# Optimization experiments

Hardware: AMD Instinct MI355X
Metric: run time of the kernel (lower is better)

The kernel has to match this reference:

```python
import jax, jax.numpy as jnp
import numpy as np

N, NUM_CLASSES, FEAT_DIM = 32768, 395, 512


def setup_inputs() -> dict:
    key = jax.random.key(0)
    k1, k2, k3, k4 = jax.random.split(key, 4)
    modal1_inputs = jax.random.normal(k1, (N, FEAT_DIM), dtype=jnp.float32)
    modal2_inputs = jax.random.normal(k2, (N, FEAT_DIM), dtype=jnp.float32)
    targets = jax.random.randint(k3, (N,), 0, NUM_CLASSES)
    # learned centers parameter: torch.rand -> uniform [0, 1)
    centers = jax.random.uniform(k4, (NUM_CLASSES, FEAT_DIM), dtype=jnp.float32)
    return {
        "modal1_inputs": modal1_inputs,
        "modal2_inputs": modal2_inputs,
        "centers": centers,
        "targets": targets,
    }


def _smooth_l1(a, b):
    # SmoothL1Loss with default beta=1.0, reduction='mean'
    d = jnp.abs(a - b)
    return jnp.mean(jnp.where(d < 1.0, 0.5 * d * d, d - 0.5))


def reference(modal1_inputs, modal2_inputs, centers, targets):
    num_classes = centers.shape[0]
    # Per-label mean (the original O(N^2) loop is exactly a segment mean
    # gathered back per sample).
    ones = jnp.ones((targets.shape[0],), dtype=modal1_inputs.dtype)
    counts = jax.ops.segment_sum(ones, targets, num_segments=num_classes)
    counts = jnp.maximum(counts, 1.0)  # empty classes never gathered
    sum1 = jax.ops.segment_sum(modal1_inputs, targets, num_segments=num_classes)
    sum2 = jax.ops.segment_sum(modal2_inputs, targets, num_segments=num_classes)
    centersR = (sum1 / counts[:, None])[targets]  # [N, D]
    centersT = (sum2 / counts[:, None])[targets]  # [N, D]
    gathered_centers = centers[targets]           # [N, D]
    loss = _smooth_l1(centersR, gathered_centers) + _smooth_l1(centersT, gathered_centers)
    return loss
```

## Files before the change

### kernel.cpp

```cpp
#include <hip/hip_runtime.h>

#define NS 32768
#define NC 395
#define FD 512
#define NEL (NC * FD)

#define RS 16
#define CT 16
#define COLS 32
#define ROWS_PB (NS / RS)
#define NW 8
#define LCAP 384

__device__ float g_part[2 * RS * NC * FD];
__device__ int   g_hist[RS * NC];

__global__ __launch_bounds__(512, 4)
void k_stream(const float* __restrict__ m1, const float* __restrict__ m2,
              const int* __restrict__ targets, float* __restrict__ out)
{
    const int bid = blockIdx.x;
    const int ct  = bid & (CT - 1);
    const int mod = (bid >> 4) & 1;
    const int rs  = bid >> 5;
    const int t   = threadIdx.x;
    const int w   = t >> 6;
    const int lane = t & 63;
    const int col  = lane & 31;
    const bool lo  = lane < 32;

    __shared__ float acc[NC * COLS];
    __shared__ int   lists[NW * LCAP];

    for (int i = t; i < NC * COLS; i += 512) acc[i] = 0.f;
    if (bid == 0 && t == 0) out[0] = 0.f;

    const int* tgt = targets + rs * ROWS_PB;
    int* mylist = &lists[w * LCAP];
    int cnt = 0;
    int nxt = tgt[lane];
    for (int it = 0; it < ROWS_PB / 64; ++it) {
        int c = nxt;
        if (it + 1 < ROWS_PB / 64) nxt = tgt[(it + 1) * 64 + lane];
        bool pred = ((c & 7) == w);
        unsigned long long mask = __ballot(pred);
        int pos = (int)__popcll(mask & ((1ull << lane) - 1ull));
        if (pred && cnt + pos < LCAP)
            mylist[cnt + pos] = (it * 64 + lane) | (c << 12);
        cnt += (int)__popcll(mask);
    }
    if (cnt > LCAP) cnt = LCAP;
    __syncthreads();

    const float* src = (mod ? m2 : m1) + (size_t)rs * ROWS_PB * FD + ct * COLS;
    const int npairs = (cnt + 1) >> 1;
    const int nbat   = (npairs + 3) >> 2;

    int ca0, cb0, ca1, cb1, ca2, cb2, ca3, cb3;
    int da0, db0, da1, db1, da2, db2, da3, db3;
    float v0, v1, v2, v3, u0, u1, u2, u3;

#define LOADP(CA, CB, V, P)                                              \
    {   int p_ = (P);                                                    \
        if (p_ < npairs) {                                               \
            int j0 = p_ << 1;                                            \
            int2 ee = *reinterpret_cast<const int2*>(&mylist[j0]);       \
            bool hb = (j0 + 1) < cnt;                                    \
            CA = ee.x >> 12;                                             \
            CB = hb ? (ee.y >> 12) : -1;                                 \
            int e = lo ? ee.x : (hb ? ee.y : ee.x);                      \
            V = src[(size_t)(e & 0xFFF) * FD + col];                     \
        } else { CA = -1; CB = -1; V = 0.f; }                            \
    }

#define RMWP(CA, CB, V)                                                  \
    if (CA >= 0) {                                                       \
        float v_ = V;                                                    \
        if (CA == CB) v_ += __shfl_xor(v_, 32, 64);                      \
        int cc = lo ? CA : CB;                                           \
        if (cc >= 0) acc[cc * COLS + col] += v_;                         \
    }

    LOADP(ca0, cb0, v0, 0) LOADP(ca1, cb1, v1, 1)
    LOADP(ca2, cb2, v2, 2) LOADP(ca3, cb3, v3, 3)
    for (int b = 1; b < nbat; ++b) {
        int pb = b << 2;
        LOADP(da0, db0, u0, pb)     LOADP(da1, db1, u1, pb + 1)
        LOADP(da2, db2, u2, pb + 2) LOADP(da3, db3, u3, pb + 3)
        RMWP(ca0, cb0, v0) RMWP(ca1, cb1, v1)
        RMWP(ca2, cb2, v2) RMWP(ca3, cb3, v3)
        ca0=da0; cb0=db0; v0=u0; ca1=da1; cb1=db1; v1=u1;
        ca2=da2; cb2=db2; v2=u2; ca3=da3; cb3=db3; v3=u3;
    }
    RMWP(ca0, cb0, v0) RMWP(ca1, cb1, v1)
    RMWP(ca2, cb2, v2) RMWP(ca3, cb3, v3)
#undef LOADP
#undef RMWP
    __syncthreads();

    float4* dst = reinterpret_cast<float4*>(g_part)
                + (size_t)(mod * RS + rs) * (NEL / 4) + ct * (COLS / 4);
    for (int i = t; i < NC * (COLS / 4); i += 512) {
        int cls = i >> 3, c4 = i & 7;
        const float* ap = &acc[cls * COLS + c4 * 4];
        float4 vv; vv.x = ap[0]; vv.y = ap[1]; vv.z = ap[2]; vv.w = ap[3];
        dst[(size_t)cls * (FD / 4) + c4] = vv;
    }

    if (ct == 0 && mod == 0) {
        __syncthreads();
        int* h = reinterpret_cast<int*>(acc);
        for (int i = t; i < NC; i += 512) h[i] = 0;
        __syncthreads();
        for (int i = t; i < ROWS_PB; i += 512) atomicAdd(&h[tgt[i]], 1);
        __syncthreads();
        for (int i = t; i < NC; i += 512) g_hist[rs * NC + i] = h[i];
    }
}

__device__ __forceinline__ float smooth_l1(float d) {
    d = fabsf(d);
    return d < 1.0f ? 0.5f * d * d : d - 0.5f;
}

__device__ __forceinline__ void f4add(float4& a, const float4 b) {
    a.x += b.x; a.y += b.y; a.z += b.z; a.w += b.w;
}

__global__ __launch_bounds__(256)
void k_loss(const float* __restrict__ centers, float* __restrict__ out) {
    __shared__ float scnt[NC];
    int t = threadIdx.x;
    for (int c = t; c < NC; c += 256) {
        int s = 0;
        #pragma unroll
        for (int k = 0; k < RS; ++k) s += g_hist[k * NC + c];
        scnt[c] = (float)s;
    }
    __syncthreads();

    const float4* ctr4  = reinterpret_cast<const float4*>(centers);
    const float4* part4 = reinterpret_cast<const float4*>(g_part);
    const int NE4 = NEL / 4;
    float val = 0.f;
    for (int g = blockIdx.x * 256 + t; g < NE4; g += gridDim.x * 256) {
        int cls = g >> 7;
        float cnt = scnt[cls];
        if (cnt > 0.f) {
            float4 s1 = make_float4(0,0,0,0), s2 = make_float4(0,0,0,0);
            #pragma unroll
            for (int k = 0; k < RS; ++k) {
                f4add(s1, part4[(size_t)k        * NE4 + g]);
                f4add(s2, part4[(size_t)(RS + k) * NE4 + g]);
            }
            float4 c4 = ctr4[g];
            float inv = 1.f / cnt;
            val += cnt * (smooth_l1(s1.x * inv - c4.x) + smooth_l1(s2.x * inv - c4.x)
                        + smooth_l1(s1.y * inv - c4.y) + smooth_l1(s2.y * inv - c4.y)
                        + smooth_l1(s1.z * inv - c4.z) + smooth_l1(s2.z * inv - c4.z)
                        + smooth_l1(s1.w * inv - c4.w) + smooth_l1(s2.w * inv - c4.w));
        }
    }

    for (int off = 32; off > 0; off >>= 1)
        val += __shfl_down(val, off, 64);
    __shared__ float wsum[4];
    int lane = t & 63, wid = t >> 6;
    if (lane == 0) wsum[wid] = val;
    __syncthreads();
    if (t == 0) {
        float sm = wsum[0] + wsum[1] + wsum[2] + wsum[3];
        atomicAdd(out, sm * 5.9604644775390625e-08f);
    }
}

extern "C" void kernel_launch(void* const* d_in, const int* in_sizes, int n_in,
                              void* d_out, int out_size, void* d_ws, size_t ws_size,
                              hipStream_t stream) {
    const float* m1 = (const float*)d_in[0];
    const float* m2 = (const float*)d_in[1];
    const float* centers = (const float*)d_in[2];
    const int* targets = (const int*)d_in[3];
    float* out = (float*)d_out;

    k_stream<<<RS * 2 * CT, 512, 0, stream>>>(m1, m2, targets, out);
    k_loss<<<200, 256, 0, stream>>>(centers, out);
}
```

Baseline: 186.0 us.

## Switch scatter-accumulate to float4 rows with in-wave conflict ranking

The per-block shared accumulation changes from scalar 32-column pairs to float4 loads, so each wave handles 8 rows of 8 float4 columns. Rows that hit the same class inside a wave are serialized by a shuffle-based rank, and the float4 slots in shared memory are swizzled by class to spread LDS banks. This aims to cut the number of load and LDS instructions per element, at the cost of extra shuffle and ballot work for duplicate detection. The loss kernel grid also doubles from 200 to 400 blocks.

```diff
diff --git a/kernel.cpp b/kernel.cpp
--- a/kernel.cpp
+++ b/kernel.cpp
@@ -8,6 +8,7 @@
 #define RS 16
 #define CT 16
 #define COLS 32
+#define CF4 8
 #define ROWS_PB (NS / RS)
 #define NW 8
 #define LCAP 384
@@ -26,13 +27,16 @@
     const int t   = threadIdx.x;
     const int w   = t >> 6;
     const int lane = t & 63;
-    const int col  = lane & 31;
-    const bool lo  = lane < 32;
+    const int r    = lane >> 3;
+    const int c4   = lane & 7;
 
-    __shared__ float acc[NC * COLS];
-    __shared__ int   lists[NW * LCAP];
+    __shared__ float4 acc4[NC * CF4];
+    __shared__ int    lists[NW * LCAP];
 
-    for (int i = t; i < NC * COLS; i += 512) acc[i] = 0.f;
+    {
+        float4 z = make_float4(0.f, 0.f, 0.f, 0.f);
+        for (int i = t; i < NC * CF4; i += 512) acc4[i] = z;
+    }
     if (bid == 0 && t == 0) out[0] = 0.f;
 
     const int* tgt = targets + rs * ROWS_PB;
@@ -52,64 +56,70 @@
     if (cnt > LCAP) cnt = LCAP;
     __syncthreads();
 
-    const float* src = (mod ? m2 : m1) + (size_t)rs * ROWS_PB * FD + ct * COLS;
-    const int npairs = (cnt + 1) >> 1;
-    const int nbat   = (npairs + 3) >> 2;
+    const float4* sp = reinterpret_cast<const float4*>(
+        (mod ? m2 : m1) + (size_t)rs * ROWS_PB * FD) + ct * CF4 + c4;
+    const int ngroups = (cnt + 7) >> 3;
 
-    int ca0, cb0, ca1, cb1, ca2, cb2, ca3, cb3;
-    int da0, db0, da1, db1, da2, db2, da3, db3;
-    float v0, v1, v2, v3, u0, u1, u2, u3;
-
-#define LOADP(CA, CB, V, P)                                              \
-    {   int p_ = (P);                                                    \
-        if (p_ < npairs) {                                               \
-            int j0 = p_ << 1;                                            \
-            int2 ee = *reinterpret_cast<const int2*>(&mylist[j0]);       \
-            bool hb = (j0 + 1) < cnt;                                    \
-            CA = ee.x >> 12;                                             \
-            CB = hb ? (ee.y >> 12) : -1;                                 \
-            int e = lo ? ee.x : (hb ? ee.y : ee.x);                      \
-            V = src[(size_t)(e & 0xFFF) * FD + col];                     \
-        } else { CA = -1; CB = -1; V = 0.f; }                            \
+#define LOADG(CLS, V, G)                                                 \
+    {   int g_ = (G);                                                    \
+        CLS = -1; V = make_float4(0.f, 0.f, 0.f, 0.f);                   \
+        if (g_ < ngroups) {                                              \
+            int e_   = mylist[g_ * 8 + r];        \
+            bool a_  = (g_ * 8 + r) < cnt;                               \
+            int idx_ = a_ ? (e_ & 0xFFF) : 0;                            \
+            CLS      = a_ ? (e_ >> 12) : -1;                             \
+            V        = sp[idx_ * 128];            \
+        }                                                                \
     }
 
-#define RMWP(CA, CB, V)                                                  \
-    if (CA >= 0) {                                                       \
-        float v_ = V;                                                    \
-        if (CA == CB) v_ += __shfl_xor(v_, 32, 64);                      \
-        int cc = lo ? CA : CB;                                           \
-        if (cc >= 0) acc[cc * COLS + col] += v_;                         \
+#define RMWG(CLS, V)                                                     \
+    {   int cls_ = CLS;                                                  \
+        int rank_ = 0;                                                   \
+        _Pragma("unroll")                                                \
+        for (int d_ = 1; d_ < 8; ++d_) {                                 \
+            int cu_ = __shfl_up(cls_, 8 * d_, 64);                       \
+            rank_ += (r >= d_ && cu_ == cls_) ? 1 : 0;                   \
+        }                                                                \
+        for (int k_ = 0; k_ < 8; ++k_) {                                 \
+            if (k_ > 0 && !__any(rank_ >= k_)) break;                    \
+            if (cls_ >= 0 && rank_ == k_) {                              \
+                int a_ = cls_ * 8 + ((c4 + (cls_ >> 3)) & 7);            \
+                float4 o_ = acc4[a_];                                    \
+                o_.x += V.x; o_.y += V.y; o_.z += V.z; o_.w += V.w;      \
+                acc4[a_] = o_;                                           \
+            }                                                            \
+        }                                                                \
     }
 
-    LOADP(ca0, cb0, v0, 0) LOADP(ca1, cb1, v1, 1)
-    LOADP(ca2, cb2, v2, 2) LOADP(ca3, cb3, v3, 3)
+    int cls0, cls1, cls2, cls3, cn0, cn1, cn2, cn3;
+    float4 v0, v1, v2, v3, u0, u1, u2, u3;
+
+    LOADG(cls0, v0, 0) LOADG(cls1, v1, 1) LOADG(cls2, v2, 2) LOADG(cls3, v3, 3)
+    const int nbat = (ngroups + 3) >> 2;
     for (int b = 1; b < nbat; ++b) {
-        int pb = b << 2;
-        LOADP(da0, db0, u0, pb)     LOADP(da1, db1, u1, pb + 1)
-        LOADP(da2, db2, u2, pb + 2) LOADP(da3, db3, u3, pb + 3)
-        RMWP(ca0, cb0, v0) RMWP(ca1, cb1, v1)
-        RMWP(ca2, cb2, v2) RMWP(ca3, cb3, v3)
-        ca0=da0; cb0=db0; v0=u0; ca1=da1; cb1=db1; v1=u1;
-        ca2=da2; cb2=db2; v2=u2; ca3=da3; cb3=db3; v3=u3;
+        int gb = b << 2;
+        LOADG(cn0, u0, gb)     LOADG(cn1, u1, gb + 1)
+        LOADG(cn2, u2, gb + 2) LOADG(cn3, u3, gb + 3)
+        RMWG(cls0, v0) RMWG(cls1, v1) RMWG(cls2, v2) RMWG(cls3, v3)
+        cls0 = cn0; v0 = u0; cls1 = cn1; v1 = u1;
+        cls2 = cn2; v2 = u2; cls3 = cn3; v3 = u3;
     }
-    RMWP(ca0, cb0, v0) RMWP(ca1, cb1, v1)
-    RMWP(ca2, cb2, v2) RMWP(ca3, cb3, v3)
-#undef LOADP
-#undef RMWP
+    RMWG(cls0, v0) RMWG(cls1, v1) RMWG(cls2, v2) RMWG(cls3, v3)
+#undef LOADG
+#undef RMWG
     __syncthreads();
 
     float4* dst = reinterpret_cast<float4*>(g_part)
-                + (size_t)(mod * RS + rs) * (NEL / 4) + ct * (COLS / 4);
-    for (int i = t; i < NC * (COLS / 4); i += 512) {
-        int cls = i >> 3, c4 = i & 7;
-        const float* ap = &acc[cls * COLS + c4 * 4];
-        float4 vv; vv.x = ap[0]; vv.y = ap[1]; vv.z = ap[2]; vv.w = ap[3];
-        dst[(size_t)cls * (FD / 4) + c4] = vv;
+                + (size_t)(mod * RS + rs) * (NEL / 4) + ct * CF4;
+    for (int i = t; i < NC * CF4; i += 512) {
+        int cls = i >> 3, cc = i & 7;
+        float4 vv = acc4[cls * 8 + ((cc + (cls >> 3)) & 7)];
+        dst[(size_t)cls * (FD / 4) + cc] = vv;
     }
 
     if (ct == 0 && mod == 0) {
         __syncthreads();
-        int* h = reinterpret_cast<int*>(acc);
+        int* h = reinterpret_cast<int*>(acc4);
         for (int i = t; i < NC; i += 512) h[i] = 0;
         __syncthreads();
         for (int i = t; i < ROWS_PB; i += 512) atomicAdd(&h[tgt[i]], 1);
@@ -184,5 +194,5 @@
     float* out = (float*)d_out;
 
     k_stream<<<RS * 2 * CT, 512, 0, stream>>>(m1, m2, targets, out);
-    k_loss<<<200, 256, 0, stream>>>(centers, out);
+    k_loss<<<400, 256, 0, stream>>>(centers, out);
 }
```

Result: no change. 186.2 us (+0.1%).
